# Performance work log

Measured on AMD Instinct MI355X. Metric: run time of the kernel, lower is better.

The kernel has to match this reference:

```python
import jax, jax.numpy as jnp
import numpy as np
import math

HID, NH, NKV, HD = 2048, 16, 4, 128
GROUPS = NH // NKV

def fq(x, bits, axis=None):
    # symmetric fake-quant with straight-through rounding; per-tensor unless axis given
    qmax = 2.0 ** (bits - 1) - 1.0
    if axis is None:
        amax = jnp.max(jnp.abs(x))
    else:
        amax = jnp.max(jnp.abs(x), axis=axis, keepdims=True)
    scale = jnp.maximum(amax, 1e-8) / qmax
    q = jnp.clip(jnp.round(x / scale), -qmax - 1.0, qmax) * scale
    return x + jax.lax.stop_gradient(q - x)

def dyn_quant_linear(x, W, b, w_bits=8):
    # DynamicQuantLinear: per-out-channel weight fake-quant + dynamic per-tensor 8-bit act quant
    Wq = fq(W, w_bits, axis=1)          # W: [out, in]
    xq = fq(x, 8)
    y = xq @ Wq.T
    return y + b if b is not None else y

def fq_matmul(a, b, a_bits, b_bits):
    # FakeQuantMatmul
    return jnp.einsum('hqd,hdk->hqk', fq(a, a_bits), fq(b, b_bits))

def rotate_half(x):
    x1, x2 = jnp.split(x, 2, axis=-1)
    return jnp.concatenate([-x2, x1], axis=-1)

def setup_inputs() -> dict:
    key = jax.random.key(0)
    ks = jax.random.split(key, 12)
    inp = {
        'hidden_states': jax.random.normal(ks[0], (1, 512, HID), jnp.float32),
        'cos': jax.random.uniform(ks[1], (1, 512, HD), jnp.float32),
        'sin': jax.random.uniform(ks[2], (1, 512, HD), jnp.float32),
        'cache_k': jax.random.normal(ks[3], (NKV, 8192, HD), jnp.float32),
        'cache_v': jax.random.normal(ks[4], (NKV, 8192, HD), jnp.float32),
        'mask': jnp.zeros((1, 512, 8192), jnp.float32),
        'Wq': jax.random.normal(ks[5], (NH * HD, HID), jnp.float32) * 0.02,
        'bq': jnp.zeros((NH * HD,), jnp.float32),
        'Wk': jax.random.normal(ks[6], (NKV * HD, HID), jnp.float32) * 0.02,
        'bk': jnp.zeros((NKV * HD,), jnp.float32),
        'Wv': jax.random.normal(ks[7], (NKV * HD, HID), jnp.float32) * 0.02,
        'bv': jnp.zeros((NKV * HD,), jnp.float32),
        'Wo': jax.random.normal(ks[8], (HID, NH * HD), jnp.float32) * 0.02,
    }
    return inp

def reference(hidden_states, cos, sin, cache_k, cache_v, mask, Wq, bq, Wk, bk, Wv, bv, Wo):
    # ConstFakeQuant on incoming caches
    cache_k = fq(cache_k, 8)
    cache_v = fq(cache_v, 8)
    seqlen = hidden_states.shape[1]
    x = hidden_states.reshape(seqlen, HID)  # batch_size == 1
    q = dyn_quant_linear(x, Wq, bq).reshape(seqlen, NH, HD).transpose(1, 0, 2)    # [NH,S,D]
    k = dyn_quant_linear(x, Wk, bk).reshape(seqlen, NKV, HD).transpose(1, 0, 2)   # [NKV,S,D]
    v = dyn_quant_linear(x, Wv, bv).reshape(seqlen, NKV, HD).transpose(1, 0, 2)   # [NKV,S,D]
    # RoPE
    q = q * cos + rotate_half(q) * sin
    k = k * cos + rotate_half(k) * sin
    c_len = cache_k.shape[1]
    # sliding KV cache: drop oldest seqlen, append new
    cache_k = jnp.concatenate([cache_k[:, seqlen:, :], k], axis=1)   # [NKV,c_len,D]
    cache_v = jnp.concatenate([cache_v[:, seqlen:, :], v], axis=1)
    kT = cache_k.transpose(0, 2, 1)                                   # [NKV,D,c_len]
    q4 = q.reshape(NKV, GROUPS * seqlen, HD)
    attn = fq_matmul(q4, kT, 8, 8)                                    # [NKV,G*S,c_len]
    attn = attn.reshape(NH, seqlen, c_len) / math.sqrt(HD)
    attn = attn + mask
    attn = jax.nn.softmax(attn, axis=-1)
    attn = attn.reshape(NKV, GROUPS * seqlen, c_len)
    out = fq_matmul(attn, cache_v, 8, 8)                              # sv: [NKV,G*S,D]
    out = out.reshape(NH, seqlen, HD).transpose(1, 0, 2).reshape(1, seqlen, HID)
    out = dyn_quant_linear(out.reshape(seqlen, HID), Wo, None).reshape(1, seqlen, HID)
    # cache outputs re-fake-quantized
    k_out = fq(k, 8)
    v_out = fq(v, 8)
    return (out, k_out, v_out)
```

## Files before the change

kernel.cpp:

```cpp
#include <hip/hip_runtime.h>
#include <math.h>

#define S_LEN 512
#define HID 2048
#define NH 16
#define NKV 4
#define HD 128
#define CL 8192
#define TAILN (CL - S_LEN)
#define NKO (NKV * S_LEN * HD)
#define KS1 16
#define KCH1 (CL / KS1)
#define KS2 8
#define KCH2 (CL / KS2)
#define INV_SQRT_HD 0.08838834764831845f

typedef unsigned short u16;
typedef __attribute__((ext_vector_type(8))) unsigned short u16x8;
typedef __attribute__((ext_vector_type(4))) unsigned short u16x4;
typedef __attribute__((ext_vector_type(8))) short bf16x8;
typedef __attribute__((ext_vector_type(4))) float f32x4;

enum {
  SC_AMAX_X = 0, SC_AMAX_CK, SC_AMAX_CK_TAIL, SC_AMAX_CV, SC_AMAX_CV_TAIL,
  SC_AMAX_Q, SC_AMAX_K, SC_AMAX_V, SC_AMAX_AO, SC_MIN_L,
  SC_NUM
};

__device__ __forceinline__ float warpMax64(float v) {
  #pragma unroll
  for (int o = 32; o; o >>= 1) v = fmaxf(v, __shfl_down(v, o, 64));
  return v;
}
__device__ __forceinline__ float warpMin64(float v) {
  #pragma unroll
  for (int o = 32; o; o >>= 1) v = fminf(v, __shfl_down(v, o, 64));
  return v;
}
__device__ __forceinline__ float blockMax256(float v) {
  __shared__ float sm_[4];
  __syncthreads();
  v = warpMax64(v);
  if ((threadIdx.x & 63) == 0) sm_[threadIdx.x >> 6] = v;
  __syncthreads();
  return fmaxf(fmaxf(sm_[0], sm_[1]), fmaxf(sm_[2], sm_[3]));
}
__device__ __forceinline__ float blockMin256(float v) {
  __shared__ float sn_[4];
  __syncthreads();
  v = warpMin64(v);
  if ((threadIdx.x & 63) == 0) sn_[threadIdx.x >> 6] = v;
  __syncthreads();
  return fminf(fminf(sn_[0], sn_[1]), fminf(sn_[2], sn_[3]));
}
__device__ __forceinline__ void atomicMinPosF(float* a, float v) {
  atomicMin((unsigned int*)a, __float_as_uint(v));
}
__device__ __forceinline__ float clampq(float q) {
  return fminf(fmaxf(q, -128.f), 127.f);
}
__device__ __forceinline__ u16 bf16bits(float f) {
  return (u16)(__float_as_uint(f) >> 16);
}
__device__ __forceinline__ float mk_scale(float am) {
  return fmaxf(am, 1e-8f) / 127.f;
}
__device__ __forceinline__ void gl2lds16(const u16* g, u16* l) {
  __builtin_amdgcn_global_load_lds((const __attribute__((address_space(1))) void*)g,
                                   (__attribute__((address_space(3))) void*)l, 16, 0, 0);
}

__global__ __launch_bounds__(256) void k_pre(const float* __restrict__ hidden,
                                             const float* __restrict__ ck, const float* __restrict__ cv,
                                             float* __restrict__ pp) {
  int b = blockIdx.x, tid = threadIdx.x;
  if (b < 512) {
    const int n4 = S_LEN * HID / 4;
    float m = 0.f;
    const float4* x4 = (const float4*)hidden;
    for (int i = b * 256 + tid; i < n4; i += 512 * 256) {
      float4 v = x4[i];
      m = fmaxf(m, fmaxf(fmaxf(fabsf(v.x), fabsf(v.y)), fmaxf(fabsf(v.z), fabsf(v.w))));
    }
    m = blockMax256(m);
    if (tid == 0) pp[b] = m;
  } else {
    int isv = b >= 1024;
    int bb = b - (isv ? 1024 : 512);
    const float4* x4 = (const float4*)(isv ? cv : ck);
    const int n4 = NKV * CL * HD / 4;
    float mf = 0.f, mt = 0.f;
    for (int i = bb * 256 + tid; i < n4; i += 512 * 256) {
      float4 v = x4[i];
      float a = fmaxf(fmaxf(fabsf(v.x), fabsf(v.y)), fmaxf(fabsf(v.z), fabsf(v.w)));
      mf = fmaxf(mf, a);
      int t = (i >> 5) & (CL - 1);
      if (t >= S_LEN) mt = fmaxf(mt, a);
    }
    mf = blockMax256(mf);
    mt = blockMax256(mt);
    if (tid == 0) {
      pp[512 + isv * 1024 + bb] = mf;
      pp[1024 + isv * 1024 + bb] = mt;
    }
  }
}

__global__ __launch_bounds__(256) void k_reduce_pre(const float* __restrict__ pp, float* __restrict__ sc) {
  const int slots[5] = {SC_AMAX_X, SC_AMAX_CK, SC_AMAX_CK_TAIL, SC_AMAX_CV, SC_AMAX_CV_TAIL};
  if (threadIdx.x == 0) sc[SC_MIN_L] = INFINITY;
  #pragma unroll
  for (int r = 0; r < 5; r++) {
    float v = fmaxf(pp[r * 512 + threadIdx.x], pp[r * 512 + 256 + threadIdx.x]);
    v = blockMax256(v);
    if (threadIdx.x == 0) sc[slots[r]] = v;
  }
}

__global__ __launch_bounds__(256) void k_quant_w_all(const float* __restrict__ Wq, const float* __restrict__ Wk,
                                                     const float* __restrict__ Wv, const float* __restrict__ Wo,
                                                     u16* __restrict__ WQb, u16* __restrict__ WKb,
                                                     u16* __restrict__ WVb, u16* __restrict__ WOb,
                                                     float* __restrict__ SWq, float* __restrict__ SWk,
                                                     float* __restrict__ SWv, float* __restrict__ SWo) {
  int r = blockIdx.x;
  const float* W; u16* Wb; float* SW; int row;
  if (r < 2048)      { W = Wq; Wb = WQb; SW = SWq; row = r; }
  else if (r < 2560) { W = Wk; Wb = WKb; SW = SWk; row = r - 2048; }
  else if (r < 3072) { W = Wv; Wb = WVb; SW = SWv; row = r - 2560; }
  else               { W = Wo; Wb = WOb; SW = SWo; row = r - 3072; }
  size_t base = (size_t)row * HID;
  const float4* w4 = (const float4*)(W + base);
  const int n4 = HID / 4;
  float am = 0.f;
  for (int i = threadIdx.x; i < n4; i += 256) {
    float4 v = w4[i];
    am = fmaxf(am, fmaxf(fmaxf(fabsf(v.x), fabsf(v.y)), fmaxf(fabsf(v.z), fabsf(v.w))));
  }
  am = blockMax256(am);
  float s = fmaxf(am, 1e-8f) / 127.f;
  if (threadIdx.x == 0) SW[row] = s;
  for (int i = threadIdx.x; i < n4; i += 256) {
    float4 v = w4[i];
    u16x4 o;
    o[0] = bf16bits(clampq(rintf(v.x / s)));
    o[1] = bf16bits(clampq(rintf(v.y / s)));
    o[2] = bf16bits(clampq(rintf(v.z / s)));
    o[3] = bf16bits(clampq(rintf(v.w / s)));
    *(u16x4*)(Wb + base + (size_t)i * 4) = o;
  }
}

__global__ __launch_bounds__(256) void k_quant_act_b(const float* __restrict__ in, u16* __restrict__ outp,
                                                     int n4, const float* __restrict__ sc, int axslot) {
  float s = mk_scale(sc[axslot]);
  const float4* i4 = (const float4*)in;
  for (int i = blockIdx.x * 256 + threadIdx.x; i < n4; i += gridDim.x * 256) {
    float4 v = i4[i];
    u16x4 o;
    o[0] = bf16bits(clampq(rintf(v.x / s)));
    o[1] = bf16bits(clampq(rintf(v.y / s)));
    o[2] = bf16bits(clampq(rintf(v.z / s)));
    o[3] = bf16bits(clampq(rintf(v.w / s)));
    *(u16x4*)(outp + (size_t)i * 4) = o;
  }
}

__global__ __launch_bounds__(256) void k_quant_q(const float* __restrict__ QB, u16* __restrict__ QI,
                                                 const float* __restrict__ sc) {
  int idx = blockIdx.x * 256 + threadIdx.x;
  float s = mk_scale(sc[SC_AMAX_Q]);
  int e = idx * 4;
  int srow = e >> 11, rem = e & 2047;
  int h = rem >> 7, d = rem & 127;
  float4 v = *(const float4*)&QB[e];
  u16x4 o;
  o[0] = bf16bits(clampq(rintf(v.x / s)));
  o[1] = bf16bits(clampq(rintf(v.y / s)));
  o[2] = bf16bits(clampq(rintf(v.z / s)));
  o[3] = bf16bits(clampq(rintf(v.w / s)));
  *(u16x4*)(QI + ((size_t)h * S_LEN + srow) * HD + d) = o;
}

__global__ __launch_bounds__(256) void k_gemm_qkv(const u16* __restrict__ A,
                                                  const u16* __restrict__ WQb, const u16* __restrict__ WKb,
                                                  const u16* __restrict__ WVb,
                                                  const float* __restrict__ SWq, const float* __restrict__ SWk,
                                                  const float* __restrict__ SWv,
                                                  const float* __restrict__ bq, const float* __restrict__ bk,
                                                  const float* __restrict__ bv,
                                                  const float* __restrict__ sc,
                                                  float* __restrict__ QB, float* __restrict__ KB,
                                                  float* __restrict__ VB) {
  __shared__ u16 Al[64 * 64];
  __shared__ u16 Bl[64 * 64];
  int bx = blockIdx.x;
  const u16* B; const float* SW; const float* bias; float* C; int N, c0;
  if (bx < 32)      { B = WQb; SW = SWq; bias = bq; C = QB; N = HID; c0 = bx * 64; }
  else if (bx < 40) { B = WKb; SW = SWk; bias = bk; C = KB; N = NKV * HD; c0 = (bx - 32) * 64; }
  else              { B = WVb; SW = SWv; bias = bv; C = VB; N = NKV * HD; c0 = (bx - 40) * 64; }
  int tid = threadIdx.x, lane = tid & 63, w = tid >> 6;
  int g = lane >> 4, c = lane & 15;
  int wy = w >> 1, wx = w & 1;
  int r0 = blockIdx.y * 64;
  float sx = mk_scale(sc[SC_AMAX_X]);
  f32x4 acc[2][2] = {};
  for (int k0 = 0; k0 < HID; k0 += 64) {
    __syncthreads();
    #pragma unroll
    for (int i = 0; i < 2; i++) {
      int b = tid + i * 256;
      int row = b >> 3, c8d = b & 7, c8s = c8d ^ (row & 7);
      gl2lds16(A + (size_t)(r0 + row) * HID + k0 + c8s * 8, Al + b * 8);
    }
    #pragma unroll
    for (int i = 0; i < 2; i++) {
      int b = tid + i * 256;
      int row = b >> 3, c8d = b & 7, c8s = c8d ^ (row & 7);
      gl2lds16(B + (size_t)(c0 + row) * HID + k0 + c8s * 8, Bl + b * 8);
    }
    __syncthreads();
    #pragma unroll
    for (int ks = 0; ks < 2; ks++) {
      bf16x8 af[2], bf[2];
      #pragma unroll
      for (int a = 0; a < 2; a++) {
        int row = wy * 32 + a * 16 + c;
        af[a] = *(const bf16x8*)(Al + row * 64 + (((4 * ks + g) ^ (row & 7)) * 8));
      }
      #pragma unroll
      for (int b = 0; b < 2; b++) {
        int row = wx * 32 + b * 16 + c;
        bf[b] = *(const bf16x8*)(Bl + row * 64 + (((4 * ks + g) ^ (row & 7)) * 8));
      }
      __builtin_amdgcn_s_setprio(1);
      #pragma unroll
      for (int a = 0; a < 2; a++)
        #pragma unroll
        for (int b = 0; b < 2; b++)
          acc[a][b] = __builtin_amdgcn_mfma_f32_16x16x32_bf16(af[a], bf[b], acc[a][b], 0, 0, 0);
      __builtin_amdgcn_s_setprio(0);
    }
  }
  #pragma unroll
  for (int a = 0; a < 2; a++)
    #pragma unroll
    for (int b = 0; b < 2; b++) {
      int col = c0 + wx * 32 + b * 16 + c;
      float sca = sx * SW[col];
      float bs = bias[col];
      #pragma unroll
      for (int r = 0; r < 4; r++) {
        int row = r0 + wy * 32 + a * 16 + 4 * g + r;
        C[(size_t)row * N + col] = acc[a][b][r] * sca + bs;
      }
    }
}

__global__ __launch_bounds__(256) void k_gemm_q(const u16* __restrict__ A, const u16* __restrict__ B,
                                                const float* __restrict__ SW, const float* __restrict__ sc,
                                                int axslot, float* __restrict__ C, int M, int N, int K) {
  __shared__ u16 Al[64 * 64];
  __shared__ u16 Bl[64 * 64];
  int tid = threadIdx.x, lane = tid & 63, w = tid >> 6;
  int g = lane >> 4, c = lane & 15;
  int wy = w >> 1, wx = w & 1;
  int r0 = blockIdx.y * 64, c0 = blockIdx.x * 64;
  float sx = mk_scale(sc[axslot]);
  f32x4 acc[2][2] = {};
  for (int k0 = 0; k0 < K; k0 += 64) {
    __syncthreads();
    #pragma unroll
    for (int i = 0; i < 2; i++) {
      int b = tid + i * 256;
      int row = b >> 3, c8d = b & 7, c8s = c8d ^ (row & 7);
      gl2lds16(A + (size_t)(r0 + row) * K + k0 + c8s * 8, Al + b * 8);
    }
    #pragma unroll
    for (int i = 0; i < 2; i++) {
      int b = tid + i * 256;
      int row = b >> 3, c8d = b & 7, c8s = c8d ^ (row & 7);
      gl2lds16(B + (size_t)(c0 + row) * K + k0 + c8s * 8, Bl + b * 8);
    }
    __syncthreads();
    #pragma unroll
    for (int ks = 0; ks < 2; ks++) {
      bf16x8 af[2], bf[2];
      #pragma unroll
      for (int a = 0; a < 2; a++) {
        int row = wy * 32 + a * 16 + c;
        af[a] = *(const bf16x8*)(Al + row * 64 + (((4 * ks + g) ^ (row & 7)) * 8));
      }
      #pragma unroll
      for (int b = 0; b < 2; b++) {
        int row = wx * 32 + b * 16 + c;
        bf[b] = *(const bf16x8*)(Bl + row * 64 + (((4 * ks + g) ^ (row & 7)) * 8));
      }
      __builtin_amdgcn_s_setprio(1);
      #pragma unroll
      for (int a = 0; a < 2; a++)
        #pragma unroll
        for (int b = 0; b < 2; b++)
          acc[a][b] = __builtin_amdgcn_mfma_f32_16x16x32_bf16(af[a], bf[b], acc[a][b], 0, 0, 0);
      __builtin_amdgcn_s_setprio(0);
    }
  }
  #pragma unroll
  for (int a = 0; a < 2; a++)
    #pragma unroll
    for (int b = 0; b < 2; b++) {
      int col = c0 + wx * 32 + b * 16 + c;
      float sca = sx * SW[col];
      #pragma unroll
      for (int r = 0; r < 4; r++) {
        int row = r0 + wy * 32 + a * 16 + 4 * g + r;
        C[(size_t)row * N + col] = acc[a][b][r] * sca;
      }
    }
}

__global__ __launch_bounds__(256) void k_rope_amax(float* __restrict__ QB, float* __restrict__ KB,
                                                   const float* __restrict__ VB,
                                                   const float* __restrict__ cosb, const float* __restrict__ sinb,
                                                   float* __restrict__ PR) {
  const int nQ = S_LEN * NH * 64;
  const int nK = S_LEN * NKV * 64;
  int idx = blockIdx.x * 256 + threadIdx.x;
  float am = 0.f;
  if (idx < nQ) {
    int s = idx >> 10, rem = idx & 1023, h = rem >> 6, d = rem & 63;
    float c1 = cosb[s * HD + d], s1 = sinb[s * HD + d];
    float c2 = cosb[s * HD + d + 64], s2 = sinb[s * HD + d + 64];
    float* p = &QB[(size_t)s * (NH * HD) + h * HD + d];
    float x1 = p[0], x2 = p[64];
    float y1 = x1 * c1 - x2 * s1;
    float y2 = x2 * c2 + x1 * s2;
    p[0] = y1; p[64] = y2;
    am = fmaxf(fabsf(y1), fabsf(y2));
  } else if (idx < nQ + nK) {
    int j = idx - nQ;
    int s = j >> 8, rem = j & 255, h = rem >> 6, d = rem & 63;
    float c1 = cosb[s * HD + d], s1 = sinb[s * HD + d];
    float c2 = cosb[s * HD + d + 64], s2 = sinb[s * HD + d + 64];
    float* p = &KB[(size_t)s * (NKV * HD) + h * HD + d];
    float x1 = p[0], x2 = p[64];
    float y1 = x1 * c1 - x2 * s1;
    float y2 = x2 * c2 + x1 * s2;
    p[0] = y1; p[64] = y2;
    am = fmaxf(fabsf(y1), fabsf(y2));
  } else {
    int j = idx - nQ - nK;
    float4 v = ((const float4*)VB)[j];
    am = fmaxf(fmaxf(fabsf(v.x), fabsf(v.y)), fmaxf(fabsf(v.z), fabsf(v.w)));
  }
  am = blockMax256(am);
  if (threadIdx.x == 0) PR[blockIdx.x] = am;
}

__global__ __launch_bounds__(256) void k_reduce_rope(const float* __restrict__ PR, float* __restrict__ sc) {
  float v = 0.f;
  #pragma unroll
  for (int i = 0; i < 8; i++) v = fmaxf(v, PR[threadIdx.x + 256 * i]);
  v = blockMax256(v);
  if (threadIdx.x == 0) sc[SC_AMAX_Q] = v;
  v = fmaxf(PR[2048 + threadIdx.x], PR[2048 + 256 + threadIdx.x]);
  v = blockMax256(v);
  if (threadIdx.x == 0) sc[SC_AMAX_K] = v;
  v = PR[2560 + threadIdx.x];
  v = blockMax256(v);
  if (threadIdx.x == 0) sc[SC_AMAX_V] = v;
}

__global__ __launch_bounds__(256) void k_build_cache2(const float* __restrict__ ck, const float* __restrict__ cv,
                                                      const float* __restrict__ KB, const float* __restrict__ VB,
                                                      u16* __restrict__ KCb, u16* __restrict__ VCb,
                                                      u16* __restrict__ VT, float* __restrict__ dout,
                                                      const float* __restrict__ sc) {
  __shared__ u16 T[64][140];
  int b = blockIdx.x;
  int isv = b >= NKV * 128;
  int bb = b - isv * NKV * 128;
  int kvh = bb >> 7, tb = bb & 127;
  float s1 = mk_scale(sc[isv ? SC_AMAX_CV : SC_AMAX_CK]);
  float tq = fminf(rintf(sc[isv ? SC_AMAX_CV_TAIL : SC_AMAX_CK_TAIL] / s1), 127.f) * s1;
  float s2 = fmaxf(fmaxf(tq, sc[isv ? SC_AMAX_V : SC_AMAX_K]), 1e-8f) / 127.f;
  float so = mk_scale(sc[isv ? SC_AMAX_V : SC_AMAX_K]);
  const float* cache = isv ? cv : ck;
  const float* fresh = isv ? VB : KB;
  u16* Cb = isv ? VCb : KCb;
  int tid = threadIdx.x;
  int t0 = tb * 64;
  #pragma unroll
  for (int i = 0; i < 8; i++) {
    int idx = tid + i * 256;
    int t = idx >> 5, d4 = (idx & 31) << 2;
    int tt = t0 + t;
    float4 x;
    float q0_, q1_, q2_, q3_;
    if (tt < TAILN) {
      x = *(const float4*)&cache[((size_t)kvh * CL + tt + S_LEN) * HD + d4];
      q0_ = clampq(rintf(clampq(rintf(x.x / s1)) * s1 / s2));
      q1_ = clampq(rintf(clampq(rintf(x.y / s1)) * s1 / s2));
      q2_ = clampq(rintf(clampq(rintf(x.z / s1)) * s1 / s2));
      q3_ = clampq(rintf(clampq(rintf(x.w / s1)) * s1 / s2));
    } else {
      x = *(const float4*)&fresh[(size_t)(tt - TAILN) * (NKV * HD) + kvh * HD + d4];
      q0_ = clampq(rintf(x.x / s2));
      q1_ = clampq(rintf(x.y / s2));
      q2_ = clampq(rintf(x.z / s2));
      q3_ = clampq(rintf(x.w / s2));
      float4 o;
      o.x = clampq(rintf(x.x / so)) * so;
      o.y = clampq(rintf(x.y / so)) * so;
      o.z = clampq(rintf(x.z / so)) * so;
      o.w = clampq(rintf(x.w / so)) * so;
      *(float4*)&dout[(size_t)S_LEN * HID + (size_t)isv * NKO +
                      ((size_t)kvh * S_LEN + (tt - TAILN)) * HD + d4] = o;
    }
    u16x4 ov;
    ov[0] = bf16bits(q0_); ov[1] = bf16bits(q1_); ov[2] = bf16bits(q2_); ov[3] = bf16bits(q3_);
    *(u16x4*)(Cb + ((size_t)kvh * CL + tt) * HD + d4) = ov;
    if (isv) *(u16x4*)&T[t][d4] = ov;
  }
  if (isv) {
    __syncthreads();
    #pragma unroll
    for (int i = 0; i < 4; i++) {
      int j = tid + i * 256;
      int d = j >> 3, tc = (j & 7) << 3;
      u16x8 v;
      #pragma unroll
      for (int k = 0; k < 8; k++) v[k] = T[tc + k][d];
      *(u16x8*)(VT + ((size_t)kvh * HD + d) * CL + t0 + tc) = v;
    }
  }
}

__global__ __launch_bounds__(256) void k_mattn1(const u16* __restrict__ QI, const u16* __restrict__ KCb,
                                                const float* __restrict__ mask, const float* __restrict__ sc,
                                                float* __restrict__ PM, float* __restrict__ PL) {
  __shared__ u16 Kl[64 * HD];
  int bid = blockIdx.x;
  int wki = (bid & 7) * (NH * 8 * KS1 / 8) + (bid >> 3);
  int kc = wki >> 7, rem2 = wki & 127, qb = rem2 >> 4, h = rem2 & 15, kv = h >> 2;
  int tid = threadIdx.x, lane = tid & 63, wv = tid >> 6, g = lane >> 4, c = lane & 15;
  float sq  = mk_scale(sc[SC_AMAX_Q]);
  float sck = mk_scale(sc[SC_AMAX_CK]);
  float tqk = fminf(rintf(sc[SC_AMAX_CK_TAIL] / sck), 127.f) * sck;
  float skn = fmaxf(fmaxf(tqk, sc[SC_AMAX_K]), 1e-8f) / 127.f;
  float sscale = sq * skn * INV_SQRT_HD;
  int q0 = qb * 64 + wv * 16;
  bf16x8 qf[4];
  {
    const u16* qrow = QI + ((size_t)h * S_LEN + q0 + c) * HD + g * 8;
    #pragma unroll
    for (int ds = 0; ds < 4; ds++) qf[ds] = *(const bf16x8*)(qrow + 32 * ds);
  }
  float m[4], l[4];
  #pragma unroll
  for (int r = 0; r < 4; r++) { m[r] = -INFINITY; l[r] = 0.f; }
  int qlane = q0 + 4 * g;
  int kbase0 = kc * KCH1;
  const u16* Kg = KCb + (size_t)kv * CL * HD;
  for (int kb = 0; kb < KCH1; kb += 64) {
    int kbase = kbase0 + kb;
    __syncthreads();
    #pragma unroll
    for (int i = 0; i < 4; i++) {
      int b = tid + i * 256;
      int row = b >> 4, c8d = b & 15, c8s = c8d ^ (row & 7);
      gl2lds16(Kg + (size_t)(kbase + row) * HD + c8s * 8, Kl + b * 8);
    }
    __syncthreads();
    f32x4 sc4[4];
    #pragma unroll
    for (int kf = 0; kf < 4; kf++) {
      f32x4 s4 = {0.f, 0.f, 0.f, 0.f};
      int krow = kf * 16 + c;
      __builtin_amdgcn_s_setprio(1);
      #pragma unroll
      for (int ds = 0; ds < 4; ds++) {
        bf16x8 kf8 = *(const bf16x8*)(Kl + krow * HD + (((4 * ds + g) ^ (krow & 7)) * 8));
        s4 = __builtin_amdgcn_mfma_f32_16x16x32_bf16(qf[ds], kf8, s4, 0, 0, 0);
      }
      __builtin_amdgcn_s_setprio(0);
      sc4[kf] = s4;
    }
    #pragma unroll
    for (int r = 0; r < 4; r++) {
      const float* mr = mask + (size_t)(qlane + r) * CL + kbase;
      float v0 = fmaf(sc4[0][r], sscale, mr[c]);
      float v1 = fmaf(sc4[1][r], sscale, mr[16 + c]);
      float v2 = fmaf(sc4[2][r], sscale, mr[32 + c]);
      float v3 = fmaf(sc4[3][r], sscale, mr[48 + c]);
      float tmax = fmaxf(fmaxf(v0, v1), fmaxf(v2, v3));
      float nm = fmaxf(m[r], tmax);
      float e0 = __expf(v0 - nm), e1 = __expf(v1 - nm);
      float e2 = __expf(v2 - nm), e3 = __expf(v3 - nm);
      float f = __expf(m[r] - nm);
      l[r] = fmaf(l[r], f, (e0 + e1) + (e2 + e3));
      m[r] = nm;
    }
  }
  #pragma unroll
  for (int r = 0; r < 4; r++) {
    #pragma unroll
    for (int off = 1; off < 16; off <<= 1) {
      float om = __shfl_xor(m[r], off, 64);
      float ol = __shfl_xor(l[r], off, 64);
      float nm = fmaxf(m[r], om);
      l[r] = l[r] * __expf(m[r] - nm) + ol * __expf(om - nm);
      m[r] = nm;
    }
  }
  if (c == 0) {
    size_t base = ((size_t)kc * NH + h) * S_LEN + qlane;
    #pragma unroll
    for (int r = 0; r < 4; r++) { PM[base + r] = m[r]; PL[base + r] = l[r]; }
  }
}

__global__ __launch_bounds__(256) void k_merge4(const float* __restrict__ PM, const float* __restrict__ PL,
                                                float* __restrict__ MLm, float* __restrict__ MLl, float* sc) {
  int idx = blockIdx.x * 256 + threadIdx.x;
  const int st = NH * S_LEN;
  float m = PM[idx];
  #pragma unroll
  for (int p = 1; p < KS1; p++) m = fmaxf(m, PM[p * st + idx]);
  float l = 0.f;
  #pragma unroll
  for (int p = 0; p < KS1; p++) l += PL[p * st + idx] * __expf(PM[p * st + idx] - m);
  MLm[idx] = m; MLl[idx] = l;
  float lm = blockMin256(l);
  if (threadIdx.x == 0) atomicMinPosF(&sc[SC_MIN_L], lm);
}

__global__ __launch_bounds__(256) void k_mattn2(const u16* __restrict__ QI, const u16* __restrict__ KCb,
                                                const u16* __restrict__ VT, const float* __restrict__ mask,
                                                const float* __restrict__ sc, const float* __restrict__ MLm,
                                                const float* __restrict__ MLl, float* __restrict__ AOp) {
  __shared__ u16 Kl[64 * HD];
  __shared__ u16 Vl[HD * 64];
  __shared__ u16 Pl[4 * 16 * 64];
  int bid = blockIdx.x;
  int wki = (bid & 7) * (NH * 8 * KS2 / 8) + (bid >> 3);
  int kc = wki >> 7, rem2 = wki & 127, qb = rem2 >> 4, h = rem2 & 15, kv = h >> 2;
  int tid = threadIdx.x, lane = tid & 63, wv = tid >> 6, g = lane >> 4, c = lane & 15;
  float sq  = mk_scale(sc[SC_AMAX_Q]);
  float sck = mk_scale(sc[SC_AMAX_CK]);
  float tqk = fminf(rintf(sc[SC_AMAX_CK_TAIL] / sck), 127.f) * sck;
  float skn = fmaxf(fmaxf(tqk, sc[SC_AMAX_K]), 1e-8f) / 127.f;
  float sscale = sq * skn * INV_SQRT_HD;
  float scv = mk_scale(sc[SC_AMAX_CV]);
  float tqv = fminf(rintf(sc[SC_AMAX_CV_TAIL] / scv), 127.f) * scv;
  float svn = fmaxf(fmaxf(tqv, sc[SC_AMAX_V]), 1e-8f) / 127.f;
  float sp  = mk_scale(1.0f / sc[SC_MIN_L]);
  float rsp = 1.0f / sp;
  float psv = sp * svn;
  int q0 = qb * 64 + wv * 16;
  bf16x8 qf[4];
  {
    const u16* qrow = QI + ((size_t)h * S_LEN + q0 + c) * HD + g * 8;
    #pragma unroll
    for (int ds = 0; ds < 4; ds++) qf[ds] = *(const bf16x8*)(qrow + 32 * ds);
  }
  int qlane = q0 + 4 * g;
  float mreg[4], invl[4];
  #pragma unroll
  for (int r = 0; r < 4; r++) {
    mreg[r] = MLm[h * S_LEN + qlane + r];
    invl[r] = 1.0f / MLl[h * S_LEN + qlane + r];
  }
  f32x4 acc[8] = {};
  const u16* Kg = KCb + (size_t)kv * CL * HD;
  const u16* Vg = VT + (size_t)kv * HD * CL;
  int kbase0 = kc * KCH2;
  u16* Pw = Pl + wv * 1024;
  for (int kb = 0; kb < KCH2; kb += 64) {
    int kbase = kbase0 + kb;
    __syncthreads();
    #pragma unroll
    for (int i = 0; i < 4; i++) {
      int b = tid + i * 256;
      int row = b >> 4, c8d = b & 15, c8s = c8d ^ (row & 7);
      gl2lds16(Kg + (size_t)(kbase + row) * HD + c8s * 8, Kl + b * 8);
    }
    #pragma unroll
    for (int i = 0; i < 4; i++) {
      int b = tid + i * 256;
      int row = b >> 3, c8d = b & 7, c8s = c8d ^ (row & 7);
      gl2lds16(Vg + (size_t)row * CL + kbase + c8s * 8, Vl + b * 8);
    }
    __syncthreads();
    #pragma unroll
    for (int kf = 0; kf < 4; kf++) {
      f32x4 s4 = {0.f, 0.f, 0.f, 0.f};
      int krow = kf * 16 + c;
      __builtin_amdgcn_s_setprio(1);
      #pragma unroll
      for (int ds = 0; ds < 4; ds++) {
        bf16x8 kf8 = *(const bf16x8*)(Kl + krow * HD + (((4 * ds + g) ^ (krow & 7)) * 8));
        s4 = __builtin_amdgcn_mfma_f32_16x16x32_bf16(qf[ds], kf8, s4, 0, 0, 0);
      }
      __builtin_amdgcn_s_setprio(0);
      int key = kbase + kf * 16 + c;
      #pragma unroll
      for (int r = 0; r < 4; r++) {
        float v = fmaf(s4[r], sscale, mask[(size_t)(qlane + r) * CL + key]);
        float p = __expf(v - mreg[r]) * invl[r];
        float pi = fminf(rintf(p * rsp), 127.f);
        int prow = 4 * g + r, pcol = kf * 16 + c;
        Pw[prow * 64 + (pcol ^ ((prow & 7) << 3))] = bf16bits(pi);
      }
    }
    asm volatile("s_waitcnt lgkmcnt(0)" ::: "memory");
    __builtin_amdgcn_sched_barrier(0);
    bf16x8 pa[2];
    #pragma unroll
    for (int s = 0; s < 2; s++)
      pa[s] = *(const bf16x8*)(Pw + c * 64 + ((32 * s + 8 * g) ^ ((c & 7) << 3)));
    __builtin_amdgcn_s_setprio(1);
    #pragma unroll
    for (int dt = 0; dt < 8; dt++) {
      #pragma unroll
      for (int s = 0; s < 2; s++) {
        int drow = dt * 16 + c;
        bf16x8 vf = *(const bf16x8*)(Vl + drow * 64 + (((4 * s + g) ^ (drow & 7)) * 8));
        acc[dt] = __builtin_amdgcn_mfma_f32_16x16x32_bf16(pa[s], vf, acc[dt], 0, 0, 0);
      }
    }
    __builtin_amdgcn_s_setprio(0);
  }
  float* outp = AOp + (size_t)kc * S_LEN * HID;
  #pragma unroll
  for (int dt = 0; dt < 8; dt++)
    #pragma unroll
    for (int r = 0; r < 4; r++)
      outp[(size_t)(qlane + r) * HID + h * HD + dt * 16 + c] = acc[dt][r] * psv;
}

__global__ __launch_bounds__(256) void k_combine_ao(const float* __restrict__ AOp, float* __restrict__ AO,
                                                    float* __restrict__ PA) {
  int idx = blockIdx.x * 256 + threadIdx.x;
  const int st = S_LEN * HID / 4;
  const f32x4* p4 = (const f32x4*)AOp;
  f32x4 a = p4[idx];
  #pragma unroll
  for (int p = 1; p < KS2; p++) {
    f32x4 b = p4[p * st + idx];
    a = a + b;
  }
  *((f32x4*)AO + idx) = a;
  float am = fmaxf(fmaxf(fabsf(a[0]), fabsf(a[1])), fmaxf(fabsf(a[2]), fabsf(a[3])));
  am = blockMax256(am);
  if (threadIdx.x == 0) PA[blockIdx.x] = am;
}

__global__ __launch_bounds__(256) void k_reduce_ao(const float* __restrict__ PA, float* __restrict__ sc) {
  float v = 0.f;
  #pragma unroll
  for (int i = 0; i < 4; i++) v = fmaxf(v, PA[threadIdx.x + 256 * i]);
  v = blockMax256(v);
  if (threadIdx.x == 0) sc[SC_AMAX_AO] = v;
}

extern "C" void kernel_launch(void* const* d_in, const int* in_sizes, int n_in,
                              void* d_out, int out_size, void* d_ws, size_t ws_size,
                              hipStream_t stream) {
  const float* hidden = (const float*)d_in[0];
  const float* cosb   = (const float*)d_in[1];
  const float* sinb   = (const float*)d_in[2];
  const float* cachek = (const float*)d_in[3];
  const float* cachev = (const float*)d_in[4];
  const float* mask   = (const float*)d_in[5];
  const float* Wq     = (const float*)d_in[6];
  const float* bq     = (const float*)d_in[7];
  const float* Wk     = (const float*)d_in[8];
  const float* bk     = (const float*)d_in[9];
  const float* Wv     = (const float*)d_in[10];
  const float* bv     = (const float*)d_in[11];
  const float* Wo     = (const float*)d_in[12];
  float* out = (float*)d_out;

  char* base = (char*)d_ws;
  auto alloc = [&](size_t bytes) { char* p = base; base += (bytes + 255) & ~(size_t)255; return p; };

  float* SC  = (float*)alloc(64 * 4);
  float* PP  = (float*)alloc(2560 * 4);
  float* PR  = (float*)alloc(2816 * 4);
  float* PA  = (float*)alloc(1024 * 4);
  float* SWq = (float*)alloc(HID * 4);
  float* SWk = (float*)alloc(NKV * HD * 4);
  float* SWv = (float*)alloc(NKV * HD * 4);
  float* SWo = (float*)alloc(HID * 4);
  u16* XI    = (u16*)alloc((size_t)S_LEN * HID * 2);
  u16* WQb   = (u16*)alloc((size_t)HID * HID * 2);
  u16* WKb   = (u16*)alloc((size_t)NKV * HD * HID * 2);
  u16* WVb   = (u16*)alloc((size_t)NKV * HD * HID * 2);
  u16* WOb   = (u16*)alloc((size_t)HID * HID * 2);
  float* QB  = (float*)alloc((size_t)S_LEN * HID * 4);
  float* KB  = (float*)alloc((size_t)S_LEN * NKV * HD * 4);
  float* VB  = (float*)alloc((size_t)S_LEN * NKV * HD * 4);
  u16* KCb   = (u16*)alloc((size_t)NKV * CL * HD * 2);
  u16* VCb   = (u16*)alloc((size_t)NKV * CL * HD * 2);
  u16* VT    = (u16*)alloc((size_t)NKV * HD * CL * 2);
  u16* QI    = (u16*)alloc((size_t)NH * S_LEN * HD * 2);
  float* PM  = (float*)alloc((size_t)KS1 * NH * S_LEN * 4);
  float* PL  = (float*)alloc((size_t)KS1 * NH * S_LEN * 4);
  float* MLm = (float*)alloc((size_t)NH * S_LEN * 4);
  float* MLl = (float*)alloc((size_t)NH * S_LEN * 4);
  float* AOp = (float*)alloc((size_t)KS2 * S_LEN * HID * 4);
  float* AO  = (float*)alloc((size_t)S_LEN * HID * 4);
  u16* AOi   = (u16*)alloc((size_t)S_LEN * HID * 2);

  k_pre<<<1536, 256, 0, stream>>>(hidden, cachek, cachev, PP);
  k_reduce_pre<<<1, 256, 0, stream>>>(PP, SC);
  k_quant_w_all<<<5120, 256, 0, stream>>>(Wq, Wk, Wv, Wo, WQb, WKb, WVb, WOb, SWq, SWk, SWv, SWo);
  k_quant_act_b<<<1024, 256, 0, stream>>>(hidden, XI, S_LEN * HID / 4, SC, SC_AMAX_X);
  {
    dim3 g(48, S_LEN / 64);
    k_gemm_qkv<<<g, 256, 0, stream>>>(XI, WQb, WKb, WVb, SWq, SWk, SWv, bq, bk, bv, SC, QB, KB, VB);
  }
  k_rope_amax<<<2816, 256, 0, stream>>>(QB, KB, VB, cosb, sinb, PR);
  k_reduce_rope<<<1, 256, 0, stream>>>(PR, SC);
  k_build_cache2<<<NKV * 128 * 2, 256, 0, stream>>>(cachek, cachev, KB, VB, KCb, VCb, VT, out, SC);
  k_quant_q<<<1024, 256, 0, stream>>>(QB, QI, SC);
  k_mattn1<<<NH * 8 * KS1, 256, 0, stream>>>(QI, KCb, mask, SC, PM, PL);
  k_merge4<<<NH * S_LEN / 256, 256, 0, stream>>>(PM, PL, MLm, MLl, SC);
  k_mattn2<<<NH * 8 * KS2, 256, 0, stream>>>(QI, KCb, VT, mask, SC, MLm, MLl, AOp);
  k_combine_ao<<<1024, 256, 0, stream>>>(AOp, AO, PA);
  k_reduce_ao<<<1, 256, 0, stream>>>(PA, SC);
  k_quant_act_b<<<1024, 256, 0, stream>>>(AO, AOi, S_LEN * HID / 4, SC, SC_AMAX_AO);
  {
    dim3 g(HID / 64, S_LEN / 64);
    k_gemm_q<<<g, 256, 0, stream>>>(AOi, WOb, SWo, SC, SC_AMAX_AO, out, S_LEN, HID, HID);
  }
  (void)in_sizes; (void)n_in; (void)out_size; (void)ws_size;
}
```

Baseline: 225.7 us.

## Double-buffer K/V LDS tiles in attention kernels and drop setprio hints

Both attention passes now keep two LDS buffers for the K (and V) tiles. The next tile's global-to-LDS copy is issued before computing on the current one, with a single barrier per iteration, so load latency is meant to hide behind the MFMA and softmax work. The s_setprio hints around MFMA sections are removed from the GEMM and attention kernels. The softmax normalization and the P quantization scale are folded into one per-row multiplier. The extra LDS buffers roughly double shared memory per block in the second attention kernel, which can lower occupancy.

```diff
diff --git a/kernel.cpp b/kernel.cpp
--- a/kernel.cpp
+++ b/kernel.cpp
@@ -233,13 +233,11 @@
         int row = wx * 32 + b * 16 + c;
         bf[b] = *(const bf16x8*)(Bl + row * 64 + (((4 * ks + g) ^ (row & 7)) * 8));
       }
-      __builtin_amdgcn_s_setprio(1);
       #pragma unroll
       for (int a = 0; a < 2; a++)
         #pragma unroll
         for (int b = 0; b < 2; b++)
           acc[a][b] = __builtin_amdgcn_mfma_f32_16x16x32_bf16(af[a], bf[b], acc[a][b], 0, 0, 0);
-      __builtin_amdgcn_s_setprio(0);
     }
   }
   #pragma unroll
@@ -296,13 +294,11 @@
         int row = wx * 32 + b * 16 + c;
         bf[b] = *(const bf16x8*)(Bl + row * 64 + (((4 * ks + g) ^ (row & 7)) * 8));
       }
-      __builtin_amdgcn_s_setprio(1);
       #pragma unroll
       for (int a = 0; a < 2; a++)
         #pragma unroll
         for (int b = 0; b < 2; b++)
           acc[a][b] = __builtin_amdgcn_mfma_f32_16x16x32_bf16(af[a], bf[b], acc[a][b], 0, 0, 0);
-      __builtin_amdgcn_s_setprio(0);
     }
   }
   #pragma unroll
@@ -439,7 +435,7 @@
 __global__ __launch_bounds__(256) void k_mattn1(const u16* __restrict__ QI, const u16* __restrict__ KCb,
                                                 const float* __restrict__ mask, const float* __restrict__ sc,
                                                 float* __restrict__ PM, float* __restrict__ PL) {
-  __shared__ u16 Kl[64 * HD];
+  __shared__ u16 Kl[2][64 * HD];
   int bid = blockIdx.x;
   int wki = (bid & 7) * (NH * 8 * KS1 / 8) + (bid >> 3);
   int kc = wki >> 7, rem2 = wki & 127, qb = rem2 >> 4, h = rem2 & 15, kv = h >> 2;
@@ -462,28 +458,30 @@
   int qlane = q0 + 4 * g;
   int kbase0 = kc * KCH1;
   const u16* Kg = KCb + (size_t)kv * CL * HD;
-  for (int kb = 0; kb < KCH1; kb += 64) {
-    int kbase = kbase0 + kb;
-    __syncthreads();
+  auto stage = [&](int buf, int kbase) {
     #pragma unroll
     for (int i = 0; i < 4; i++) {
       int b = tid + i * 256;
       int row = b >> 4, c8d = b & 15, c8s = c8d ^ (row & 7);
-      gl2lds16(Kg + (size_t)(kbase + row) * HD + c8s * 8, Kl + b * 8);
-    }
-    __syncthreads();
+      gl2lds16(Kg + (size_t)(kbase + row) * HD + c8s * 8, Kl[buf] + b * 8);
+    }
+  };
+  stage(0, kbase0);
+  __syncthreads();
+  int cur = 0;
+  for (int kb = 0; kb < KCH1; kb += 64) {
+    int kbase = kbase0 + kb;
+    if (kb + 64 < KCH1) stage(cur ^ 1, kbase + 64);
     f32x4 sc4[4];
     #pragma unroll
     for (int kf = 0; kf < 4; kf++) {
       f32x4 s4 = {0.f, 0.f, 0.f, 0.f};
       int krow = kf * 16 + c;
-      __builtin_amdgcn_s_setprio(1);
       #pragma unroll
       for (int ds = 0; ds < 4; ds++) {
-        bf16x8 kf8 = *(const bf16x8*)(Kl + krow * HD + (((4 * ds + g) ^ (krow & 7)) * 8));
+        bf16x8 kf8 = *(const bf16x8*)(Kl[cur] + krow * HD + (((4 * ds + g) ^ (krow & 7)) * 8));
         s4 = __builtin_amdgcn_mfma_f32_16x16x32_bf16(qf[ds], kf8, s4, 0, 0, 0);
       }
-      __builtin_amdgcn_s_setprio(0);
       sc4[kf] = s4;
     }
     #pragma unroll
@@ -501,6 +499,8 @@
       l[r] = fmaf(l[r], f, (e0 + e1) + (e2 + e3));
       m[r] = nm;
     }
+    __syncthreads();
+    cur ^= 1;
   }
   #pragma unroll
   for (int r = 0; r < 4; r++) {
@@ -539,8 +539,8 @@
                                                 const u16* __restrict__ VT, const float* __restrict__ mask,
                                                 const float* __restrict__ sc, const float* __restrict__ MLm,
                                                 const float* __restrict__ MLl, float* __restrict__ AOp) {
-  __shared__ u16 Kl[64 * HD];
-  __shared__ u16 Vl[HD * 64];
+  __shared__ u16 Kl[2][64 * HD];
+  __shared__ u16 Vl[2][HD * 64];
   __shared__ u16 Pl[4 * 16 * 64];
   int bid = blockIdx.x;
   int wki = (bid & 7) * (NH * 8 * KS2 / 8) + (bid >> 3);
@@ -565,50 +565,51 @@
     for (int ds = 0; ds < 4; ds++) qf[ds] = *(const bf16x8*)(qrow + 32 * ds);
   }
   int qlane = q0 + 4 * g;
-  float mreg[4], invl[4];
+  float mreg[4], cvl[4];
   #pragma unroll
   for (int r = 0; r < 4; r++) {
     mreg[r] = MLm[h * S_LEN + qlane + r];
-    invl[r] = 1.0f / MLl[h * S_LEN + qlane + r];
+    cvl[r] = rsp / MLl[h * S_LEN + qlane + r];
   }
   f32x4 acc[8] = {};
   const u16* Kg = KCb + (size_t)kv * CL * HD;
   const u16* Vg = VT + (size_t)kv * HD * CL;
   int kbase0 = kc * KCH2;
   u16* Pw = Pl + wv * 1024;
-  for (int kb = 0; kb < KCH2; kb += 64) {
-    int kbase = kbase0 + kb;
-    __syncthreads();
+  auto stage = [&](int buf, int kbase) {
     #pragma unroll
     for (int i = 0; i < 4; i++) {
       int b = tid + i * 256;
       int row = b >> 4, c8d = b & 15, c8s = c8d ^ (row & 7);
-      gl2lds16(Kg + (size_t)(kbase + row) * HD + c8s * 8, Kl + b * 8);
+      gl2lds16(Kg + (size_t)(kbase + row) * HD + c8s * 8, Kl[buf] + b * 8);
     }
     #pragma unroll
     for (int i = 0; i < 4; i++) {
       int b = tid + i * 256;
       int row = b >> 3, c8d = b & 7, c8s = c8d ^ (row & 7);
-      gl2lds16(Vg + (size_t)row * CL + kbase + c8s * 8, Vl + b * 8);
-    }
-    __syncthreads();
+      gl2lds16(Vg + (size_t)row * CL + kbase + c8s * 8, Vl[buf] + b * 8);
+    }
+  };
+  stage(0, kbase0);
+  __syncthreads();
+  int cur = 0;
+  for (int kb = 0; kb < KCH2; kb += 64) {
+    int kbase = kbase0 + kb;
+    if (kb + 64 < KCH2) stage(cur ^ 1, kbase + 64);
     #pragma unroll
     for (int kf = 0; kf < 4; kf++) {
       f32x4 s4 = {0.f, 0.f, 0.f, 0.f};
       int krow = kf * 16 + c;
-      __builtin_amdgcn_s_setprio(1);
       #pragma unroll
       for (int ds = 0; ds < 4; ds++) {
-        bf16x8 kf8 = *(const bf16x8*)(Kl + krow * HD + (((4 * ds + g) ^ (krow & 7)) * 8));
+        bf16x8 kf8 = *(const bf16x8*)(Kl[cur] + krow * HD + (((4 * ds + g) ^ (krow & 7)) * 8));
         s4 = __builtin_amdgcn_mfma_f32_16x16x32_bf16(qf[ds], kf8, s4, 0, 0, 0);
       }
-      __builtin_amdgcn_s_setprio(0);
       int key = kbase + kf * 16 + c;
       #pragma unroll
       for (int r = 0; r < 4; r++) {
         float v = fmaf(s4[r], sscale, mask[(size_t)(qlane + r) * CL + key]);
-        float p = __expf(v - mreg[r]) * invl[r];
-        float pi = fminf(rintf(p * rsp), 127.f);
+        float pi = fminf(rintf(__expf(v - mreg[r]) * cvl[r]), 127.f);
         int prow = 4 * g + r, pcol = kf * 16 + c;
         Pw[prow * 64 + (pcol ^ ((prow & 7) << 3))] = bf16bits(pi);
       }
@@ -619,17 +620,17 @@
     #pragma unroll
     for (int s = 0; s < 2; s++)
       pa[s] = *(const bf16x8*)(Pw + c * 64 + ((32 * s + 8 * g) ^ ((c & 7) << 3)));
-    __builtin_amdgcn_s_setprio(1);
     #pragma unroll
     for (int dt = 0; dt < 8; dt++) {
       #pragma unroll
       for (int s = 0; s < 2; s++) {
         int drow = dt * 16 + c;
-        bf16x8 vf = *(const bf16x8*)(Vl + drow * 64 + (((4 * s + g) ^ (drow & 7)) * 8));
+        bf16x8 vf = *(const bf16x8*)(Vl[cur] + drow * 64 + (((4 * s + g) ^ (drow & 7)) * 8));
         acc[dt] = __builtin_amdgcn_mfma_f32_16x16x32_bf16(pa[s], vf, acc[dt], 0, 0, 0);
       }
     }
-    __builtin_amdgcn_s_setprio(0);
+    __syncthreads();
+    cur ^= 1;
   }
   float* outp = AOp + (size_t)kc * S_LEN * HID;
   #pragma unroll
```

Measured after the change: 210.9 us. -6.6%, faster.
